# Kernel optimization log

Measured on AMD Instinct MI355X. Metric: run time of the kernel, lower is better.

Reference implementation:

```python
import jax, jax.numpy as jnp
import numpy as np

B, C, H, W = 32, 512, 32, 32
D = C // 8

def setup_inputs() -> dict:
    key = jax.random.key(0)
    ks = jax.random.split(key, 5)
    return {
        "x": jax.random.normal(ks[0], (B, C, H, W), dtype=jnp.float32),
        "w1": jax.random.normal(ks[1], (D, C), dtype=jnp.float32) * (1.0 / np.sqrt(C)),
        "b1": jax.random.normal(ks[2], (D,), dtype=jnp.float32) * 0.01,
        "w2": jax.random.normal(ks[3], (C, C), dtype=jnp.float32) * (1.0 / np.sqrt(C)),
        "b2": jax.random.normal(ks[4], (C,), dtype=jnp.float32) * 0.01,
    }

def reference(x, w1, b1, w2, b2):
    b, c, h, w = x.shape
    n = h * w
    xf = x.reshape(b, c, n)                                   # [B,C,N]
    # 1x1 convs == channel-mixing GEMMs; conv1 is shared for q and k
    qk = jnp.einsum('bcn,dc->bdn', xf, w1) + b1[None, :, None]  # [B,D,N]
    v = jnp.einsum('bcn,oc->bon', xf, w2) + b2[None, :, None]   # [B,C,N]
    q = qk.transpose(0, 2, 1)                                 # [B,N,D]
    attn = jax.nn.softmax(jnp.einsum('bnd,bdm->bnm', q, qk), axis=-1)  # [B,N,N]
    out = jnp.einsum('bnm,bcm->bnc', attn, v)                 # [B,N,C]
    # Faithful quirk: original views [B,N,C] directly as [B,C,H,W] (no transpose)
    return x + out.reshape(b, c, h, w)
```

## Files before the change

kernel.cpp:

```cpp
#include <hip/hip_runtime.h>
#include <hip/hip_bf16.h>
#include <math.h>

#define B_ 32
#define C_ 512
#define N_ 1024
#define D_ 64
#define OPAD 640

typedef __attribute__((ext_vector_type(4))) float f32x4;
typedef __attribute__((ext_vector_type(4))) float float4v;
typedef __attribute__((ext_vector_type(8))) __bf16 bf16x8;

#define MFMA16(a, b, c) __builtin_amdgcn_mfma_f32_16x16x32_bf16((a), (b), (c), 0, 0, 0)

__device__ inline void load_lds16(const void* g, void* l) {
    __builtin_amdgcn_global_load_lds(
        (const __attribute__((address_space(1))) void*)g,
        (__attribute__((address_space(3))) void*)l, 16, 0, 0);
}

__global__ void k_cast_weights(const float* __restrict__ w1,
                               const float* __restrict__ w2,
                               __hip_bfloat16* __restrict__ Wbf) {
    int idx = blockIdx.x * 256 + threadIdx.x;
    if (idx >= OPAD * C_) return;
    int m = idx >> 9;
    int k = idx & (C_ - 1);
    float val = (m < D_) ? w1[m * C_ + k]
              : (m < D_ + C_) ? w2[(m - D_) * C_ + k] : 0.0f;
    Wbf[idx] = __float2bfloat16(val);
}

__global__ __launch_bounds__(256) void k_transpose_cast(
        const float* __restrict__ x, __hip_bfloat16* __restrict__ xT) {
    __shared__ float tile[64][68];
    int b = blockIdx.z;
    int n0 = blockIdx.x * 64;
    int c0 = blockIdx.y * 64;
    int t = threadIdx.x;
    const float* xb = x + (size_t)b * (C_ * N_);
#pragma unroll
    for (int i = 0; i < 4; i++) {
        int c = i * 16 + (t >> 4);
        int nc = (t & 15) * 4;
        *(float4v*)&tile[c][nc] =
            *(const float4v*)(xb + (size_t)(c0 + c) * N_ + n0 + nc);
    }
    __syncthreads();
    __hip_bfloat16* xTb = xT + (size_t)b * (N_ * C_);
#pragma unroll
    for (int i = 0; i < 2; i++) {
        int n = i * 32 + (t >> 3);
        int cs = (t & 7) * 8;
        alignas(16) __hip_bfloat16 tmp[8];
#pragma unroll
        for (int j = 0; j < 8; j++)
            tmp[j] = __float2bfloat16(tile[cs + j][n]);
        *(bf16x8*)(xTb + (size_t)(n0 + n) * C_ + c0 + cs) = *(bf16x8*)tmp;
    }
}

__global__ __launch_bounds__(256) void k_gemm_qkv(
        const __hip_bfloat16* __restrict__ Wbf,
        const __hip_bfloat16* __restrict__ xT,
        const float* __restrict__ b1, const float* __restrict__ b2,
        __hip_bfloat16* __restrict__ qkT, __hip_bfloat16* __restrict__ v) {
    __shared__ __hip_bfloat16 As[128 * 64];
    __shared__ __hip_bfloat16 Bs[128 * 64];
    __shared__ __hip_bfloat16 epi[4][16][72];
    int b = blockIdx.z;
    int t = threadIdx.x;
    int wave = t >> 6, lane = t & 63, lr = lane & 15, quad = lane >> 4;
    int wm = wave >> 1, wn = wave & 1;
    int m_blk = blockIdx.y * 128;
    int n_blk = blockIdx.x * 128;
    const __hip_bfloat16* xTb = xT + (size_t)b * (N_ * C_);

    f32x4 acc[4][4] = {};
    for (int kk = 0; kk < C_; kk += 64) {
#pragma unroll
        for (int i = 0; i < 4; i++) {
            int id = i * 256 + t;
            int r = id >> 3, cx = id & 7;
            int gc = cx ^ (r & 7);
            load_lds16(Wbf + (size_t)(m_blk + r) * C_ + kk + gc * 8, &As[id * 8]);
            load_lds16(xTb + (size_t)(n_blk + r) * C_ + kk + gc * 8, &Bs[id * 8]);
        }
        __syncthreads();
#pragma unroll
        for (int h = 0; h < 2; h++) {
            bf16x8 af[4], bfr[4];
#pragma unroll
            for (int i = 0; i < 4; i++) {
                int ra = wm * 64 + i * 16 + lr;
                int rb = wn * 64 + i * 16 + lr;
                int q = h * 4 + quad;
                af[i]  = *(const bf16x8*)&As[ra * 64 + (q ^ (lr & 7)) * 8];
                bfr[i] = *(const bf16x8*)&Bs[rb * 64 + (q ^ (lr & 7)) * 8];
            }
#pragma unroll
            for (int mt = 0; mt < 4; mt++)
#pragma unroll
                for (int nt = 0; nt < 4; nt++)
                    acc[mt][nt] = MFMA16(af[mt], bfr[nt], acc[mt][nt]);
        }
        __syncthreads();
    }

#pragma unroll
    for (int mt = 0; mt < 4; mt++) {
        int m_frag = m_blk + wm * 64 + mt * 16;
        if (m_frag >= D_ + C_) continue;
        int m0 = m_frag + quad * 4;
        if (m_frag < D_) {
#pragma unroll
            for (int nt = 0; nt < 4; nt++) {
                int n = n_blk + wn * 64 + nt * 16 + lr;
                alignas(8) __hip_bfloat16 tmp[4];
#pragma unroll
                for (int r = 0; r < 4; r++)
                    tmp[r] = __float2bfloat16(acc[mt][nt][r] + b1[m0 + r]);
                *reinterpret_cast<short4*>(qkT + ((size_t)b * N_ + n) * D_ + m0) =
                    *reinterpret_cast<short4*>(tmp);
            }
        } else {
#pragma unroll
            for (int nt = 0; nt < 4; nt++) {
#pragma unroll
                for (int r = 0; r < 4; r++) {
                    int c = m0 - D_ + r;
                    epi[wave][quad * 4 + r][nt * 16 + lr] =
                        __float2bfloat16(acc[mt][nt][r] + b2[c]);
                }
            }
            int cbase = m_frag - D_;
            int row = lane >> 2;
#pragma unroll
            for (int it = 0; it < 2; it++) {
                int col = it * 32 + (lane & 3) * 8;
                bf16x8 frag = *(const bf16x8*)&epi[wave][row][col];
                *(bf16x8*)(v + (size_t)(b * C_ + cbase + row) * N_
                             + n_blk + wn * 64 + col) = frag;
            }
        }
    }
}

__global__ __launch_bounds__(256) void k_fused_attn(
        const __hip_bfloat16* __restrict__ qkT,
        const __hip_bfloat16* __restrict__ v,
        const float* __restrict__ x, float* __restrict__ out) {
    __shared__ char smem[40960];
    __hip_bfloat16* Ks = (__hip_bfloat16*)smem;
    __hip_bfloat16* Vs = (__hip_bfloat16*)(smem + 8192);
    __hip_bfloat16* Ps = (__hip_bfloat16*)(smem + 24576);
    float* Obuf = (float*)smem;
    __shared__ float Rs[128];

    int b = blockIdx.z;
    int t = threadIdx.x;
    int wave = t >> 6, lane = t & 63, lr = lane & 15, quad = lane >> 4;
    int wm = wave >> 1, wn = wave & 1;
    int n_blk = blockIdx.y * 128;
    int c_blk = blockIdx.x * 128;
    const __hip_bfloat16* qb = qkT + (size_t)b * (N_ * D_);
    const __hip_bfloat16* vb = v + (size_t)b * (C_ * N_);

    union bfu { bf16x8 v; __hip_bfloat16 h[8]; };
    bf16x8 bq[2][2];
    float shift[2];
#pragma unroll
    for (int nj = 0; nj < 2; nj++) {
        int n = n_blk + wave * 32 + nj * 16 + lr;
#pragma unroll
        for (int dh = 0; dh < 2; dh++)
            bq[nj][dh] = *(const bf16x8*)(qb + (size_t)n * D_ + dh * 32 + quad * 8);
        float sq = 0.f;
#pragma unroll
        for (int dh = 0; dh < 2; dh++) {
            bfu u; u.v = bq[nj][dh];
#pragma unroll
            for (int j = 0; j < 8; j++) {
                float qv = __bfloat162float(u.h[j]);
                sq += qv * qv;
            }
        }
        sq += __shfl_xor(sq, 16);
        sq += __shfl_xor(sq, 32);
        shift[nj] = sq;
    }

    f32x4 acc[4][4] = {};
    float rsum[2] = {0.f, 0.f};

    for (int kk = 0; kk < N_; kk += 64) {
#pragma unroll
        for (int i = 0; i < 2; i++) {
            int id = i * 256 + t;
            int r = id >> 3, cx = id & 7;
            int gc = cx ^ (r & 7);
            load_lds16(qb + (size_t)(kk + r) * D_ + gc * 8, &Ks[id * 8]);
        }
#pragma unroll
        for (int i = 0; i < 4; i++) {
            int id = i * 256 + t;
            int r = id >> 3, cx = id & 7;
            int gc = cx ^ (r & 7);
            load_lds16(vb + (size_t)(c_blk + r) * N_ + kk + gc * 8, &Vs[id * 8]);
        }
        __syncthreads();

#pragma unroll
        for (int mi = 0; mi < 4; mi++) {
            int m = mi * 16 + lr;
            bf16x8 ak0 = *(const bf16x8*)&Ks[m * 64 + ((quad) ^ (lr & 7)) * 8];
            bf16x8 ak1 = *(const bf16x8*)&Ks[m * 64 + ((4 + quad) ^ (lr & 7)) * 8];
#pragma unroll
            for (int nj = 0; nj < 2; nj++) {
                f32x4 s = {};
                s = MFMA16(ak0, bq[nj][0], s);
                s = MFMA16(ak1, bq[nj][1], s);
                alignas(8) __hip_bfloat16 tmp[4];
#pragma unroll
                for (int r = 0; r < 4; r++) {
                    float e = __expf(s[r] - shift[nj]);
                    rsum[nj] += e;
                    tmp[r] = __float2bfloat16(e);
                }
                int n = wave * 32 + nj * 16 + lr;
                int cx = mi * 2 + (quad >> 1);
                int slot = cx ^ (lr & 7);
                *(short4*)&Ps[n * 64 + slot * 8 + (quad & 1) * 4] =
                    *(short4*)tmp;
            }
        }
        __syncthreads();

#pragma unroll
        for (int h = 0; h < 2; h++) {
            bf16x8 af[4], bfr[4];
#pragma unroll
            for (int i = 0; i < 4; i++) {
                int ra = wm * 64 + i * 16 + lr;
                int rb = wn * 64 + i * 16 + lr;
                int q = h * 4 + quad;
                af[i]  = *(const bf16x8*)&Ps[ra * 64 + (q ^ (lr & 7)) * 8];
                bfr[i] = *(const bf16x8*)&Vs[rb * 64 + (q ^ (lr & 7)) * 8];
            }
#pragma unroll
            for (int mt = 0; mt < 4; mt++)
#pragma unroll
                for (int nt = 0; nt < 4; nt++)
                    acc[mt][nt] = MFMA16(af[mt], bfr[nt], acc[mt][nt]);
        }
        __syncthreads();
    }

    rsum[0] += __shfl_xor(rsum[0], 16);
    rsum[0] += __shfl_xor(rsum[0], 32);
    rsum[1] += __shfl_xor(rsum[1], 16);
    rsum[1] += __shfl_xor(rsum[1], 32);
    if (quad == 0) {
        Rs[wave * 32 + lr]      = 1.0f / rsum[0];
        Rs[wave * 32 + 16 + lr] = 1.0f / rsum[1];
    }
    __syncthreads();

    const float* xb = x + (size_t)b * (N_ * C_);
    float* ob = out + (size_t)b * (N_ * C_);
#pragma unroll
    for (int h = 0; h < 2; h++) {
        if (wm == h) {
#pragma unroll
            for (int mt = 0; mt < 4; mt++)
#pragma unroll
                for (int nt = 0; nt < 4; nt++)
#pragma unroll
                    for (int r = 0; r < 4; r++)
                        Obuf[(mt * 16 + quad * 4 + r) * 128 + wn * 64 + nt * 16 + lr] =
                            acc[mt][nt][r];
        }
        __syncthreads();
#pragma unroll
        for (int i = 0; i < 8; i++) {
            int id = i * 256 + t;
            int rl = id >> 5;
            int c4 = (id & 31) * 4;
            int n = n_blk + h * 64 + rl;
            float ri = Rs[h * 64 + rl];
            float4v o = *(const float4v*)&Obuf[rl * 128 + c4];
            size_t gidx = (size_t)n * C_ + c_blk + c4;
            float4v xv = *(const float4v*)(xb + gidx);
            float4v res;
            res.x = xv.x + ri * o.x;
            res.y = xv.y + ri * o.y;
            res.z = xv.z + ri * o.z;
            res.w = xv.w + ri * o.w;
            *(float4v*)(ob + gidx) = res;
        }
        __syncthreads();
    }
}

extern "C" void kernel_launch(void* const* d_in, const int* in_sizes, int n_in,
                              void* d_out, int out_size, void* d_ws, size_t ws_size,
                              hipStream_t stream) {
    const float* x  = (const float*)d_in[0];
    const float* w1 = (const float*)d_in[1];
    const float* b1 = (const float*)d_in[2];
    const float* w2 = (const float*)d_in[3];
    const float* b2 = (const float*)d_in[4];
    float* out = (float*)d_out;

    char* ws = (char*)d_ws;
    size_t off = 0;
    __hip_bfloat16* Wbf = (__hip_bfloat16*)(ws + off); off += (size_t)OPAD * C_ * 2;
    __hip_bfloat16* xT  = (__hip_bfloat16*)(ws + off); off += (size_t)B_ * N_ * C_ * 2;
    __hip_bfloat16* qkT = (__hip_bfloat16*)(ws + off); off += (size_t)B_ * N_ * D_ * 2;
    __hip_bfloat16* v   = (__hip_bfloat16*)(ws + off); off += (size_t)B_ * C_ * N_ * 2;

    hipLaunchKernelGGL(k_cast_weights, dim3((OPAD * C_ + 255) / 256), dim3(256), 0, stream,
                       w1, w2, Wbf);
    hipLaunchKernelGGL(k_transpose_cast, dim3(N_ / 64, C_ / 64, B_), dim3(256), 0, stream,
                       x, xT);
    hipLaunchKernelGGL(k_gemm_qkv, dim3(N_ / 128, OPAD / 128, B_), dim3(256), 0, stream,
                       Wbf, xT, b1, b2, qkT, v);
    hipLaunchKernelGGL(k_fused_attn, dim3(C_ / 128, N_ / 128, B_), dim3(256), 0, stream,
                       qkT, v, x, out);
}
```

Baseline: 235.5 us.

## Compute full channel width per attention block to avoid recomputing softmax

The fused attention kernel now covers all 512 channels for each 128-row query tile with 512 threads, where before it tiled 128 channels per block. Previously the QK^T scores and exponentials were recomputed for each of the four channel blocks, so this removes that redundant work. It needs much more LDS (about 88KB for the V tile), 128 accumulator registers per thread and a grid of only 256 blocks, which may lower occupancy and leave the GPU underfilled.

```diff
diff --git a/kernel.cpp b/kernel.cpp
--- a/kernel.cpp
+++ b/kernel.cpp
@@ -147,39 +147,36 @@
     }
 }
 
-__global__ __launch_bounds__(256) void k_fused_attn(
+__global__ __launch_bounds__(512, 2) void k_fused_attn(
         const __hip_bfloat16* __restrict__ qkT,
         const __hip_bfloat16* __restrict__ v,
         const float* __restrict__ x, float* __restrict__ out) {
-    __shared__ char smem[40960];
+    __shared__ char smem[90112];
     __hip_bfloat16* Ks = (__hip_bfloat16*)smem;
     __hip_bfloat16* Vs = (__hip_bfloat16*)(smem + 8192);
-    __hip_bfloat16* Ps = (__hip_bfloat16*)(smem + 24576);
+    __hip_bfloat16* Ps = (__hip_bfloat16*)(smem + 73728);
     float* Obuf = (float*)smem;
     __shared__ float Rs[128];
 
-    int b = blockIdx.z;
+    int b = blockIdx.y;
     int t = threadIdx.x;
     int wave = t >> 6, lane = t & 63, lr = lane & 15, quad = lane >> 4;
-    int wm = wave >> 1, wn = wave & 1;
-    int n_blk = blockIdx.y * 128;
-    int c_blk = blockIdx.x * 128;
+    int wm = wave >> 2, wn = wave & 3;
+    int n_blk = blockIdx.x * 128;
     const __hip_bfloat16* qb = qkT + (size_t)b * (N_ * D_);
     const __hip_bfloat16* vb = v + (size_t)b * (C_ * N_);
 
     union bfu { bf16x8 v; __hip_bfloat16 h[8]; };
-    bf16x8 bq[2][2];
-    float shift[2];
-#pragma unroll
-    for (int nj = 0; nj < 2; nj++) {
-        int n = n_blk + wave * 32 + nj * 16 + lr;
-#pragma unroll
-        for (int dh = 0; dh < 2; dh++)
-            bq[nj][dh] = *(const bf16x8*)(qb + (size_t)n * D_ + dh * 32 + quad * 8);
+    bf16x8 bq[2];
+    float shift;
+    {
+        int nq = n_blk + wave * 16 + lr;
+        bq[0] = *(const bf16x8*)(qb + (size_t)nq * D_ + quad * 8);
+        bq[1] = *(const bf16x8*)(qb + (size_t)nq * D_ + 32 + quad * 8);
         float sq = 0.f;
 #pragma unroll
         for (int dh = 0; dh < 2; dh++) {
-            bfu u; u.v = bq[nj][dh];
+            bfu u; u.v = bq[dh];
 #pragma unroll
             for (int j = 0; j < 8; j++) {
                 float qv = __bfloat162float(u.h[j]);
@@ -188,26 +185,22 @@
         }
         sq += __shfl_xor(sq, 16);
         sq += __shfl_xor(sq, 32);
-        shift[nj] = sq;
-    }
-
-    f32x4 acc[4][4] = {};
-    float rsum[2] = {0.f, 0.f};
+        shift = sq;
+    }
+
+    f32x4 acc[4][8] = {};
+    float rsum = 0.f;
 
     for (int kk = 0; kk < N_; kk += 64) {
-#pragma unroll
-        for (int i = 0; i < 2; i++) {
-            int id = i * 256 + t;
-            int r = id >> 3, cx = id & 7;
-            int gc = cx ^ (r & 7);
-            load_lds16(qb + (size_t)(kk + r) * D_ + gc * 8, &Ks[id * 8]);
-        }
-#pragma unroll
-        for (int i = 0; i < 4; i++) {
-            int id = i * 256 + t;
-            int r = id >> 3, cx = id & 7;
-            int gc = cx ^ (r & 7);
-            load_lds16(vb + (size_t)(c_blk + r) * N_ + kk + gc * 8, &Vs[id * 8]);
+        {
+            int r = t >> 3, cx = t & 7, gc = cx ^ (r & 7);
+            load_lds16(qb + (size_t)(kk + r) * D_ + gc * 8, &Ks[t * 8]);
+        }
+#pragma unroll
+        for (int i = 0; i < 8; i++) {
+            int id = i * 512 + t;
+            int r = id >> 3, cx = id & 7, gc = cx ^ (r & 7);
+            load_lds16(vb + (size_t)r * N_ + kk + gc * 8, &Vs[id * 8]);
         }
         __syncthreads();
 
@@ -216,90 +209,90 @@
             int m = mi * 16 + lr;
             bf16x8 ak0 = *(const bf16x8*)&Ks[m * 64 + ((quad) ^ (lr & 7)) * 8];
             bf16x8 ak1 = *(const bf16x8*)&Ks[m * 64 + ((4 + quad) ^ (lr & 7)) * 8];
-#pragma unroll
-            for (int nj = 0; nj < 2; nj++) {
-                f32x4 s = {};
-                s = MFMA16(ak0, bq[nj][0], s);
-                s = MFMA16(ak1, bq[nj][1], s);
-                alignas(8) __hip_bfloat16 tmp[4];
-#pragma unroll
-                for (int r = 0; r < 4; r++) {
-                    float e = __expf(s[r] - shift[nj]);
-                    rsum[nj] += e;
-                    tmp[r] = __float2bfloat16(e);
-                }
-                int n = wave * 32 + nj * 16 + lr;
-                int cx = mi * 2 + (quad >> 1);
-                int slot = cx ^ (lr & 7);
-                *(short4*)&Ps[n * 64 + slot * 8 + (quad & 1) * 4] =
-                    *(short4*)tmp;
-            }
+            f32x4 s = {};
+            s = MFMA16(ak0, bq[0], s);
+            s = MFMA16(ak1, bq[1], s);
+            alignas(8) __hip_bfloat16 tmp[4];
+#pragma unroll
+            for (int r = 0; r < 4; r++) {
+                float e = __expf(s[r] - shift);
+                rsum += e;
+                tmp[r] = __float2bfloat16(e);
+            }
+            int n = wave * 16 + lr;
+            int cx2 = mi * 2 + (quad >> 1);
+            int slot = cx2 ^ (lr & 7);
+            *(short4*)&Ps[n * 64 + slot * 8 + (quad & 1) * 4] = *(short4*)tmp;
         }
         __syncthreads();
 
 #pragma unroll
         for (int h = 0; h < 2; h++) {
-            bf16x8 af[4], bfr[4];
+            bf16x8 af[4];
 #pragma unroll
             for (int i = 0; i < 4; i++) {
                 int ra = wm * 64 + i * 16 + lr;
-                int rb = wn * 64 + i * 16 + lr;
-                int q = h * 4 + quad;
-                af[i]  = *(const bf16x8*)&Ps[ra * 64 + (q ^ (lr & 7)) * 8];
-                bfr[i] = *(const bf16x8*)&Vs[rb * 64 + (q ^ (lr & 7)) * 8];
-            }
-#pragma unroll
-            for (int mt = 0; mt < 4; mt++)
-#pragma unroll
-                for (int nt = 0; nt < 4; nt++)
-                    acc[mt][nt] = MFMA16(af[mt], bfr[nt], acc[mt][nt]);
-        }
-        __syncthreads();
-    }
-
-    rsum[0] += __shfl_xor(rsum[0], 16);
-    rsum[0] += __shfl_xor(rsum[0], 32);
-    rsum[1] += __shfl_xor(rsum[1], 16);
-    rsum[1] += __shfl_xor(rsum[1], 32);
-    if (quad == 0) {
-        Rs[wave * 32 + lr]      = 1.0f / rsum[0];
-        Rs[wave * 32 + 16 + lr] = 1.0f / rsum[1];
-    }
-    __syncthreads();
+                af[i] = *(const bf16x8*)&Ps[ra * 64 + ((h * 4 + quad) ^ (lr & 7)) * 8];
+            }
+#pragma unroll
+            for (int g = 0; g < 2; g++) {
+                bf16x8 bfr[4];
+#pragma unroll
+                for (int j = 0; j < 4; j++) {
+                    int rb = wn * 128 + (g * 4 + j) * 16 + lr;
+                    bfr[j] = *(const bf16x8*)&Vs[rb * 64 + ((h * 4 + quad) ^ (lr & 7)) * 8];
+                }
+#pragma unroll
+                for (int mt = 0; mt < 4; mt++)
+#pragma unroll
+                    for (int j = 0; j < 4; j++)
+                        acc[mt][g * 4 + j] = MFMA16(af[mt], bfr[j], acc[mt][g * 4 + j]);
+            }
+        }
+        __syncthreads();
+    }
+
+    rsum += __shfl_xor(rsum, 16);
+    rsum += __shfl_xor(rsum, 32);
+    if (quad == 0) Rs[wave * 16 + lr] = 1.0f / rsum;
 
     const float* xb = x + (size_t)b * (N_ * C_);
     float* ob = out + (size_t)b * (N_ * C_);
 #pragma unroll
     for (int h = 0; h < 2; h++) {
-        if (wm == h) {
-#pragma unroll
-            for (int mt = 0; mt < 4; mt++)
-#pragma unroll
-                for (int nt = 0; nt < 4; nt++)
-#pragma unroll
-                    for (int r = 0; r < 4; r++)
-                        Obuf[(mt * 16 + quad * 4 + r) * 128 + wn * 64 + nt * 16 + lr] =
-                            acc[mt][nt][r];
-        }
-        __syncthreads();
-#pragma unroll
-        for (int i = 0; i < 8; i++) {
-            int id = i * 256 + t;
-            int rl = id >> 5;
-            int c4 = (id & 31) * 4;
-            int n = n_blk + h * 64 + rl;
-            float ri = Rs[h * 64 + rl];
-            float4v o = *(const float4v*)&Obuf[rl * 128 + c4];
-            size_t gidx = (size_t)n * C_ + c_blk + c4;
-            float4v xv = *(const float4v*)(xb + gidx);
-            float4v res;
-            res.x = xv.x + ri * o.x;
-            res.y = xv.y + ri * o.y;
-            res.z = xv.z + ri * o.z;
-            res.w = xv.w + ri * o.w;
-            *(float4v*)(ob + gidx) = res;
-        }
-        __syncthreads();
+#pragma unroll
+        for (int g = 0; g < 2; g++) {
+            __syncthreads();
+            if (wm == h && (wn >> 1) == g) {
+#pragma unroll
+                for (int mt = 0; mt < 4; mt++)
+#pragma unroll
+                    for (int nt = 0; nt < 8; nt++)
+#pragma unroll
+                        for (int r = 0; r < 4; r++)
+                            Obuf[(mt * 16 + quad * 4 + r) * 260
+                                 + (wn & 1) * 128 + nt * 16 + lr] =
+                                acc[mt][nt][r];
+            }
+            __syncthreads();
+#pragma unroll
+            for (int i = 0; i < 8; i++) {
+                int id = i * 512 + t;
+                int rl = id >> 6;
+                int c4 = (id & 63) * 4;
+                int n = n_blk + h * 64 + rl;
+                float ri = Rs[h * 64 + rl];
+                float4v o = *(const float4v*)&Obuf[rl * 260 + c4];
+                size_t gidx = (size_t)n * C_ + g * 256 + c4;
+                float4v xv = *(const float4v*)(xb + gidx);
+                float4v res;
+                res.x = xv.x + ri * o.x;
+                res.y = xv.y + ri * o.y;
+                res.z = xv.z + ri * o.z;
+                res.w = xv.w + ri * o.w;
+                *(float4v*)(ob + gidx) = res;
+            }
+        }
     }
 }
 
@@ -326,6 +319,6 @@
                        x, xT);
     hipLaunchKernelGGL(k_gemm_qkv, dim3(N_ / 128, OPAD / 128, B_), dim3(256), 0, stream,
                        Wbf, xT, b1, b2, qkT, v);
-    hipLaunchKernelGGL(k_fused_attn, dim3(C_ / 128, N_ / 128, B_), dim3(256), 0, stream,
+    hipLaunchKernelGGL(k_fused_attn, dim3(N_ / 128, B_), dim3(512), 0, stream,
                        qkT, v, x, out);
 }
```

Measured after the change: 218.3 us. 1.08x faster.
